# Kernel tuning notes

Measured on AMD Instinct MI355X. Metric: run time of the kernel, lower is better.

Reference implementation:

```python
import jax, jax.numpy as jnp
import numpy as np

VTH = 1.0          # firing threshold
SG_ALPHA = 4.0     # surrogate-gradient sharpness
TAU_MEM = 20.0

@jax.custom_vjp
def spike_fn(v):
    # Heaviside spike: 1 where membrane exceeds 0 (v is already v_mem - VTH)
    return (v > 0.0).astype(v.dtype)

def _spike_fwd(v):
    return spike_fn(v), v

def _spike_bwd(v, g):
    # sigmoid surrogate derivative: alpha * s * (1 - s)
    s = jax.nn.sigmoid(SG_ALPHA * v)
    return (g * SG_ALPHA * s * (1.0 - s),)

spike_fn.defvjp(_spike_fwd, _spike_bwd)

def lif_scan(h):
    # h: (batch, time, seq, hidden) -> spikes same shape, rate scalar
    beta = 1.0 - 1.0 / TAU_MEM  # membrane decay
    b, t, s, d = h.shape
    h_t = jnp.moveaxis(h, 1, 0)  # (time, batch, seq, hidden)

    def step(v, inp):
        v = beta * v + inp
        spk = spike_fn(v - VTH)
        v = v * (1.0 - spk)  # hard reset
        return v, spk

    v0 = jnp.zeros((b, s, d), dtype=h.dtype)
    _, spikes = jax.lax.scan(step, v0, h_t)
    spikes = jnp.moveaxis(spikes, 0, 1)  # (batch, time, seq, hidden)
    rate = spikes.mean()
    return spikes, rate

def setup_inputs() -> dict:
    key = jax.random.key(0)
    k1, k2, k3 = jax.random.split(key, 3)
    b, t, s, d = 16, 4, 256, 512
    hidden = 2048
    x = jax.random.normal(k1, (b, t, s, d), dtype=jnp.float32)
    # Kaiming-ish init so membrane inputs are O(1)
    w1 = jax.random.normal(k2, (hidden, d), dtype=jnp.float32) * (1.0 / np.sqrt(d))
    w2 = jax.random.normal(k3, (d, hidden), dtype=jnp.float32) * (1.0 / np.sqrt(hidden))
    return {"x": x, "w1": w1, "w2": w2}

def reference(x, w1, w2):
    # fc1: (b,t,s,d) @ (hidden,d)^T -> (b,t,s,hidden)
    h = jnp.einsum('btsd,hd->btsh', x, w1)
    spikes, rate = lif_scan(h)
    # fc2: (b,t,s,hidden) @ (d,hidden)^T -> (b,t,s,d)
    out = jnp.einsum('btsh,dh->btsd', spikes, w2)
    return out, rate
```

## Files before the change

kernel.cpp:

```cpp
#include <hip/hip_runtime.h>
#include <stdint.h>


typedef __attribute__((ext_vector_type(8))) short short8;
typedef __attribute__((ext_vector_type(4))) float f32x4;

#define AS1 __attribute__((address_space(1)))
#define AS3 __attribute__((address_space(3)))

__device__ __forceinline__ void load_lds16(const void* g, void* l) {
  __builtin_amdgcn_global_load_lds((const AS1 void*)g, (AS3 void*)l, 16, 0, 0);
}

__device__ __forceinline__ unsigned short f2bf(float f) {
  union { float f; unsigned u; } un; un.f = f;
  unsigned r = un.u + 0x7FFF + ((un.u >> 16) & 1);
  return (unsigned short)(r >> 16);
}
__device__ __forceinline__ float bf2f(unsigned short u) {
  union { unsigned u; float f; } un; un.u = ((unsigned)u) << 16; return un.f;
}

__global__ __launch_bounds__(256) void k0_split(
    const float* __restrict__ w2, unsigned short* __restrict__ hi,
    unsigned short* __restrict__ lo)
{
  int i = (blockIdx.x * 256 + threadIdx.x) * 4;
  float4 w = *(const float4*)&w2[i];
  unsigned short h4[4], l4[4];
  float ws[4] = {w.x, w.y, w.z, w.w};
#pragma unroll
  for (int c = 0; c < 4; ++c) {
    unsigned short h = f2bf(ws[c]);
    h4[c] = h;
    l4[c] = f2bf(ws[c] - bf2f(h));
  }
  *(ushort4*)&hi[i] = *(const ushort4*)h4;
  *(ushort4*)&lo[i] = *(const ushort4*)l4;
}

#define K1KT 32
#define SA_STR 256
#define SB_STR 128

__global__ __launch_bounds__(256, 2) void k1_gemm_lif(
    const float* __restrict__ x,
    const float* __restrict__ w1,
    unsigned short* __restrict__ spikes,
    unsigned* __restrict__ cnt_out)
{
  __shared__ float sA[K1KT * SA_STR];
  __shared__ float sB[K1KT * SB_STR];

  const int tid = threadIdx.x;
  const int tx  = tid & 15;
  const int ty  = tid >> 4;
  const int t   = ty & 3;
  const int ssg = ty >> 2;

  const int bx = blockIdx.x;
  const int b  = bx >> 2;
  const int s0 = (bx & 3) * 64;
  const int h0 = blockIdx.y * 128;

  const int u  = tid >> 3;
  const int kg = tid & 7;

  float acc[16][8];
#pragma unroll
  for (int i = 0; i < 16; ++i)
#pragma unroll
    for (int j = 0; j < 8; ++j) acc[i][j] = 0.0f;

  const int aBase  = t * 64 + ssg * 16;
  const int tXor   = 4 * t;
  const int bBase0 = tx * 4;
  const int bBase1 = 64 + tx * 4;

  for (int k0 = 0; k0 < 512; k0 += K1KT) {
    __syncthreads();

#pragma unroll
    for (int j = 0; j < 8; ++j) {
      int r  = u + 32 * j;
      int tr = r >> 6, ss = r & 63;
      size_t grow = ((size_t)(b * 4 + tr) << 8) + s0 + ss;
      float4 a = *(const float4*)&x[grow * 512 + k0 + kg * 4];
      int sl = r ^ (4 * (kg ^ tr));
      sA[(4 * kg + 0) * SA_STR + sl] = a.x;
      sA[(4 * kg + 1) * SA_STR + sl] = a.y;
      sA[(4 * kg + 2) * SA_STR + sl] = a.z;
      sA[(4 * kg + 3) * SA_STR + sl] = a.w;
    }
#pragma unroll
    for (int j = 0; j < 4; ++j) {
      int c = u + 32 * j;
      float4 wv = *(const float4*)&w1[(size_t)(h0 + c) * 512 + k0 + kg * 4];
      int sl = c ^ (4 * kg);
      sB[(4 * kg + 0) * SB_STR + sl] = wv.x;
      sB[(4 * kg + 1) * SB_STR + sl] = wv.y;
      sB[(4 * kg + 2) * SB_STR + sl] = wv.z;
      sB[(4 * kg + 3) * SB_STR + sl] = wv.w;
    }
    __syncthreads();

    for (int kk = 0; kk < K1KT; kk += 4) {
      const int aXor = kk ^ tXor;
      const int bXor = kk;
#pragma unroll
      for (int k2i = 0; k2i < 4; ++k2i) {
        const int k = kk + k2i;
        const float* aRow = &sA[k * SA_STR];
        const float* bRow = &sB[k * SB_STR];
        float4 a0 = *(const float4*)&aRow[(aBase + 0)  ^ aXor];
        float4 a1 = *(const float4*)&aRow[(aBase + 4)  ^ aXor];
        float4 a2 = *(const float4*)&aRow[(aBase + 8)  ^ aXor];
        float4 a3 = *(const float4*)&aRow[(aBase + 12) ^ aXor];
        float4 b0 = *(const float4*)&bRow[bBase0 ^ bXor];
        float4 b1 = *(const float4*)&bRow[bBase1 ^ bXor];
        float av[16] = {a0.x, a0.y, a0.z, a0.w, a1.x, a1.y, a1.z, a1.w,
                        a2.x, a2.y, a2.z, a2.w, a3.x, a3.y, a3.z, a3.w};
        float bv[8]  = {b0.x, b0.y, b0.z, b0.w, b1.x, b1.y, b1.z, b1.w};
#pragma unroll
        for (int i = 0; i < 16; ++i)
#pragma unroll
          for (int j = 0; j < 8; ++j)
            acc[i][j] = __builtin_fmaf(av[i], bv[j], acc[i][j]);
      }
    }
  }

  unsigned cnt = 0;
#pragma unroll
  for (int i = 0; i < 16; ++i) {
    unsigned short sp[8];
#pragma unroll
    for (int j = 0; j < 8; ++j) {
      float a = acc[i][j];
      float h[4];
#pragma unroll
      for (int tt = 0; tt < 4; ++tt)
        h[tt] = __shfl(a, tt * 16 + tx, 64);
      float vv = 0.0f;
      bool smine = false;
#pragma unroll
      for (int tt = 0; tt < 4; ++tt) {
        vv = __fadd_rn(__fmul_rn(0.95f, vv), h[tt]);
        bool s = vv > 1.0f;
        smine = (tt == t) ? s : smine;
        vv = s ? 0.0f : vv;
      }
      cnt += smine ? 1u : 0u;
      sp[j] = smine ? (unsigned short)0x3F80 : (unsigned short)0;
    }
    size_t grow = ((size_t)(b * 4 + t) << 8) + s0 + ssg * 16 + i;
    unsigned short* rowp = spikes + grow * 2048 + h0;
    *(ushort4*)&rowp[tx * 4]      = *(const ushort4*)&sp[0];
    *(ushort4*)&rowp[64 + tx * 4] = *(const ushort4*)&sp[4];
  }

#pragma unroll
  for (int off = 32; off; off >>= 1) cnt += __shfl_down(cnt, off);
  if ((tid & 63) == 0) atomicAdd(cnt_out, cnt);
}

__global__ __launch_bounds__(256, 2) void k2_gemm_mfma(
    const unsigned short* __restrict__ spikes,
    const unsigned short* __restrict__ w2h,
    const unsigned short* __restrict__ w2l,
    float* __restrict__ out)
{
  __shared__ alignas(16) short smA [128 * 64];
  __shared__ alignas(16) short smBh[128 * 64];
  __shared__ alignas(16) short smBl[128 * 64];

  const int tid  = threadIdx.x;
  const int lane = tid & 63;
  const int quad = lane >> 4;
  const int l15  = lane & 15;
  const int wv   = tid >> 6;
  const int wm   = wv & 1;
  const int wn   = wv >> 1;

  const size_t r0 = (size_t)blockIdx.x * 128;
  const int    d0 = blockIdx.y * 128;

  int srow[4], sg8[4];
#pragma unroll
  for (int j = 0; j < 4; ++j) {
    int gi  = j * 256 + tid;
    srow[j] = gi >> 3;
    sg8[j]  = ((gi & 7) ^ (srow[j] & 7)) * 8;
  }

  const unsigned short* ab  = spikes + r0 * 2048;
  const unsigned short* bhb = w2h + (size_t)d0 * 2048;
  const unsigned short* blb = w2l + (size_t)d0 * 2048;

  f32x4 acc[4][4] = {};

  for (int k0 = 0; k0 < 2048; k0 += 64) {
    __syncthreads();
#pragma unroll
    for (int j = 0; j < 4; ++j) {
      load_lds16(ab  + (size_t)srow[j] * 2048 + k0 + sg8[j],
                 &smA [(j * 256 + tid) * 8]);
      load_lds16(bhb + (size_t)srow[j] * 2048 + k0 + sg8[j],
                 &smBh[(j * 256 + tid) * 8]);
      load_lds16(blb + (size_t)srow[j] * 2048 + k0 + sg8[j],
                 &smBl[(j * 256 + tid) * 8]);
    }
    __syncthreads();

#pragma unroll
    for (int ks = 0; ks < 2; ++ks) {
      short8 af[4], bh[4], bl[4];
#pragma unroll
      for (int mi = 0; mi < 4; ++mi) {
        int m = wm * 64 + mi * 16 + l15;
        af[mi] = ((const short8*)smA)[m * 8 + ((ks * 4 + quad) ^ (m & 7))];
      }
#pragma unroll
      for (int ni = 0; ni < 4; ++ni) {
        int n = wn * 64 + ni * 16 + l15;
        int sl = n * 8 + ((ks * 4 + quad) ^ (n & 7));
        bh[ni] = ((const short8*)smBh)[sl];
        bl[ni] = ((const short8*)smBl)[sl];
      }
#pragma unroll
      for (int mi = 0; mi < 4; ++mi)
#pragma unroll
        for (int ni = 0; ni < 4; ++ni) {
          acc[mi][ni] = __builtin_amdgcn_mfma_f32_16x16x32_bf16(
              af[mi], bh[ni], acc[mi][ni], 0, 0, 0);
          acc[mi][ni] = __builtin_amdgcn_mfma_f32_16x16x32_bf16(
              af[mi], bl[ni], acc[mi][ni], 0, 0, 0);
        }
    }
  }

  float* ob = out + r0 * 512 + d0;
#pragma unroll
  for (int mi = 0; mi < 4; ++mi)
#pragma unroll
    for (int ni = 0; ni < 4; ++ni)
#pragma unroll
      for (int r = 0; r < 4; ++r) {
        int rr = wm * 64 + mi * 16 + quad * 4 + r;
        int cc = wn * 64 + ni * 16 + l15;
        ob[(size_t)rr * 512 + cc] = acc[mi][ni][r];
      }
}

#define KT 16
#define PADF 68

__global__ __launch_bounds__(256) void k2_gemm_valu(
    const unsigned short* __restrict__ spikes,
    const float* __restrict__ w2,
    float* __restrict__ out)
{
  __shared__ float sA[KT][PADF];
  __shared__ float sB[KT][PADF];

  const int tid = threadIdx.x;
  const int tx  = tid & 15;
  const int ty  = tid >> 4;
  const int lr  = tid >> 2;
  const int lg  = tid & 3;

  const size_t r0 = (size_t)blockIdx.x * 64;
  const int    d0 = blockIdx.y * 64;

  float acc[4][4];
#pragma unroll
  for (int i = 0; i < 4; ++i)
#pragma unroll
    for (int j = 0; j < 4; ++j) acc[i][j] = 0.0f;

  for (int k0 = 0; k0 < 2048; k0 += KT) {
    __syncthreads();
    ushort4 av = *(const ushort4*)&spikes[(r0 + lr) * 2048 + k0 + lg * 4];
    float4  bv = *(const float4*)&w2[(size_t)(d0 + lr) * 2048 + k0 + lg * 4];
    sA[lg * 4 + 0][lr] = bf2f(av.x); sA[lg * 4 + 1][lr] = bf2f(av.y);
    sA[lg * 4 + 2][lr] = bf2f(av.z); sA[lg * 4 + 3][lr] = bf2f(av.w);
    sB[lg * 4 + 0][lr] = bv.x; sB[lg * 4 + 1][lr] = bv.y;
    sB[lg * 4 + 2][lr] = bv.z; sB[lg * 4 + 3][lr] = bv.w;
    __syncthreads();

#pragma unroll
    for (int k = 0; k < KT; ++k) {
      float4 a4 = *(const float4*)&sA[k][ty * 4];
      float4 b4 = *(const float4*)&sB[k][tx * 4];
      float aa[4] = {a4.x, a4.y, a4.z, a4.w};
      float bb[4] = {b4.x, b4.y, b4.z, b4.w};
#pragma unroll
      for (int i = 0; i < 4; ++i)
#pragma unroll
        for (int j = 0; j < 4; ++j)
          acc[i][j] = __builtin_fmaf(aa[i], bb[j], acc[i][j]);
    }
  }

#pragma unroll
  for (int i = 0; i < 4; ++i) {
    float4 o = make_float4(acc[i][0], acc[i][1], acc[i][2], acc[i][3]);
    *(float4*)&out[(r0 + ty * 4 + i) * 512 + d0 + tx * 4] = o;
  }
}

__global__ void k3_rate(const unsigned* __restrict__ cnt, float* __restrict__ dst) {
  dst[0] = (float)((double)(*cnt) / 33554432.0);
}

extern "C" void kernel_launch(void* const* d_in, const int* in_sizes, int n_in,
                              void* d_out, int out_size, void* d_ws, size_t ws_size,
                              hipStream_t stream) {
  const float* x  = (const float*)d_in[0];
  const float* w1 = (const float*)d_in[1];
  const float* w2 = (const float*)d_in[2];
  float* out = (float*)d_out;

  unsigned* cnt = (unsigned*)d_ws;
  unsigned short* spikes = (unsigned short*)((char*)d_ws + 256);
  const size_t SPIKES_B = (size_t)16384 * 2048 * 2;
  unsigned short* w2h = (unsigned short*)((char*)d_ws + 256 + SPIKES_B);
  unsigned short* w2l = w2h + (size_t)512 * 2048;
  const size_t NEED_SPLIT = 256 + SPIKES_B + 2 * (size_t)512 * 2048 * 2;

  hipMemsetAsync(d_ws, 0, 256, stream);

  hipLaunchKernelGGL(k1_gemm_lif, dim3(64, 16), dim3(256), 0, stream,
                     x, w1, spikes, cnt);

  if (ws_size >= NEED_SPLIT) {
    hipLaunchKernelGGL(k0_split, dim3(1024), dim3(256), 0, stream, w2, w2h, w2l);
    hipLaunchKernelGGL(k2_gemm_mfma, dim3(128, 4), dim3(256), 0, stream,
                       spikes, w2h, w2l, out);
  } else {
    hipLaunchKernelGGL(k2_gemm_valu, dim3(256, 8), dim3(256), 0, stream,
                       spikes, w2, out);
  }

  hipLaunchKernelGGL(k3_rate, dim3(1), dim3(1), 0, stream, cnt, out + 8388608);
}
```

Baseline: 562.6 us.

## Pre-transpose x and w1 so fc1 tiles load directly into LDS

```diff
diff --git a/kernel.cpp b/kernel.cpp
--- a/kernel.cpp
+++ b/kernel.cpp
@@ -21,6 +21,29 @@
   union { unsigned u; float f; } un; un.u = ((unsigned)u) << 16; return un.f;
 }
 
+__global__ __launch_bounds__(256) void ktrans(
+    const float* __restrict__ s, float* __restrict__ d, int M, int N)
+{
+  __shared__ float t[64][68];
+  const int tx = threadIdx.x & 15, ty = threadIdx.x >> 4;
+  const size_t r0 = (size_t)blockIdx.x * 64;
+  const int    c0 = blockIdx.y * 64;
+#pragma unroll
+  for (int p = 0; p < 4; ++p) {
+    int r = ty + 16 * p;
+    float4 v = *(const float4*)&s[(r0 + r) * N + c0 + tx * 4];
+    t[tx * 4 + 0][r] = v.x; t[tx * 4 + 1][r] = v.y;
+    t[tx * 4 + 2][r] = v.z; t[tx * 4 + 3][r] = v.w;
+  }
+  __syncthreads();
+#pragma unroll
+  for (int p = 0; p < 4; ++p) {
+    int c = ty + 16 * p;
+    float4 v = *(const float4*)&t[c][tx * 4];
+    *(float4*)&d[(size_t)(c0 + c) * M + r0 + tx * 4] = v;
+  }
+}
+
 __global__ __launch_bounds__(256) void k0_split(
     const float* __restrict__ w2, unsigned short* __restrict__ hi,
     unsigned short* __restrict__ lo)
@@ -40,14 +63,126 @@
 }
 
 #define K1KT 32
+
+__global__ __launch_bounds__(256, 2) void k1_gemm_lif(
+    const float* __restrict__ xT,
+    const float* __restrict__ w1T,
+    unsigned short* __restrict__ spikes,
+    unsigned* __restrict__ cnt_out)
+{
+  __shared__ float sA[K1KT * 256];
+  __shared__ float sB[K1KT * 128];
+
+  const int tid  = threadIdx.x;
+  const int lane = tid & 63;
+  const int w    = tid >> 6;
+  const int tx   = tid & 15;
+  const int ty   = tid >> 4;
+  const int t    = ty & 3;
+  const int ssg  = ty >> 2;
+
+  const int bx = blockIdx.x;
+  const int b  = bx >> 2;
+  const int s0 = (bx & 3) * 64;
+  const int h0 = blockIdx.y * 128;
+
+  const int aT = lane >> 4;
+  const int aS = (lane & 15) * 4;
+  const int bK = lane >> 5;
+  const int bC = (lane & 31) * 4;
+
+  const float* aSrc = xT + ((size_t)(b * 4 + aT) << 8) + s0 + aS;
+  const float* bSrc = w1T + h0 + bC;
+
+  float acc[16][8];
+#pragma unroll
+  for (int i = 0; i < 16; ++i)
+#pragma unroll
+    for (int j = 0; j < 8; ++j) acc[i][j] = 0.0f;
+
+  const int aBase = t * 64 + ssg * 16;
+
+  for (int k0 = 0; k0 < 512; k0 += K1KT) {
+    __syncthreads();
+
+#pragma unroll
+    for (int j = 0; j < 8; ++j) {
+      int kr = w * 8 + j;
+      load_lds16(aSrc + (size_t)(k0 + kr) * 16384, &sA[kr * 256 + lane * 4]);
+    }
+#pragma unroll
+    for (int j = 0; j < 4; ++j) {
+      int kr = (w * 4 + j) * 2;
+      load_lds16(bSrc + (size_t)(k0 + kr + bK) * 2048,
+                 &sB[kr * 128 + lane * 4]);
+    }
+    __syncthreads();
+
+#pragma unroll
+    for (int k = 0; k < K1KT; ++k) {
+      const float* aRow = &sA[k * 256];
+      const float* bRow = &sB[k * 128];
+      float4 afr[4];
+#pragma unroll
+      for (int ig = 0; ig < 4; ++ig) {
+        int igr = (ig + t) & 3;
+        afr[igr] = *(const float4*)&aRow[aBase + 4 * igr];
+      }
+      float4 b0 = *(const float4*)&bRow[tx * 4];
+      float4 b1 = *(const float4*)&bRow[64 + tx * 4];
+      float av[16] = {afr[0].x, afr[0].y, afr[0].z, afr[0].w,
+                      afr[1].x, afr[1].y, afr[1].z, afr[1].w,
+                      afr[2].x, afr[2].y, afr[2].z, afr[2].w,
+                      afr[3].x, afr[3].y, afr[3].z, afr[3].w};
+      float bv[8]  = {b0.x, b0.y, b0.z, b0.w, b1.x, b1.y, b1.z, b1.w};
+#pragma unroll
+      for (int i = 0; i < 16; ++i)
+#pragma unroll
+        for (int j = 0; j < 8; ++j)
+          acc[i][j] = __builtin_fmaf(av[i], bv[j], acc[i][j]);
+    }
+  }
+
+  unsigned cnt = 0;
+#pragma unroll
+  for (int i = 0; i < 16; ++i) {
+    unsigned short sp[8];
+#pragma unroll
+    for (int j = 0; j < 8; ++j) {
+      float a = acc[i][j];
+      float h[4];
+#pragma unroll
+      for (int tt = 0; tt < 4; ++tt)
+        h[tt] = __shfl(a, tt * 16 + tx, 64);
+      float vv = 0.0f;
+      bool smine = false;
+#pragma unroll
+      for (int tt = 0; tt < 4; ++tt) {
+        vv = __fadd_rn(__fmul_rn(0.95f, vv), h[tt]);
+        bool s = vv > 1.0f;
+        smine = (tt == t) ? s : smine;
+        vv = s ? 0.0f : vv;
+      }
+      cnt += smine ? 1u : 0u;
+      sp[j] = smine ? (unsigned short)0x3F80 : (unsigned short)0;
+    }
+    size_t grow = ((size_t)(b * 4 + t) << 8) + s0 + ssg * 16 + i;
+    unsigned short* rowp = spikes + grow * 2048 + h0;
+    *(ushort4*)&rowp[tx * 4]      = *(const ushort4*)&sp[0];
+    *(ushort4*)&rowp[64 + tx * 4] = *(const ushort4*)&sp[4];
+  }
+
+#pragma unroll
+  for (int off = 32; off; off >>= 1) cnt += __shfl_down(cnt, off);
+  if ((tid & 63) == 0) atomicAdd(cnt_out, cnt);
+}
+
 #define SA_STR 256
 #define SB_STR 128
 
-__global__ __launch_bounds__(256, 2) void k1_gemm_lif(
-    const float* __restrict__ x,
-    const float* __restrict__ w1,
-    unsigned short* __restrict__ spikes,
-    unsigned* __restrict__ cnt_out)
+__global__ __launch_bounds__(256, 2) void k1_fb(
+    const float* __restrict__ x, const float* __restrict__ w1,
+    unsigned short* __restrict__ spikes, unsigned* __restrict__ cnt_out)
 {
   __shared__ float sA[K1KT * SA_STR];
   __shared__ float sB[K1KT * SB_STR];
@@ -79,7 +214,6 @@
 
   for (int k0 = 0; k0 < 512; k0 += K1KT) {
     __syncthreads();
-
 #pragma unroll
     for (int j = 0; j < 8; ++j) {
       int r  = u + 32 * j;
@@ -321,17 +455,33 @@
   const float* w2 = (const float*)d_in[2];
   float* out = (float*)d_out;
 
-  unsigned* cnt = (unsigned*)d_ws;
-  unsigned short* spikes = (unsigned short*)((char*)d_ws + 256);
+  char* wsb = (char*)d_ws;
+  unsigned* cnt = (unsigned*)wsb;
+  unsigned short* spikes = (unsigned short*)(wsb + 256);
   const size_t SPIKES_B = (size_t)16384 * 2048 * 2;
-  unsigned short* w2h = (unsigned short*)((char*)d_ws + 256 + SPIKES_B);
+  const size_t W2S_B    = (size_t)512 * 2048 * 2;
+  unsigned short* w2h = (unsigned short*)(wsb + 256 + SPIKES_B);
   unsigned short* w2l = w2h + (size_t)512 * 2048;
-  const size_t NEED_SPLIT = 256 + SPIKES_B + 2 * (size_t)512 * 2048 * 2;
+  float* xT  = (float*)(wsb + 256 + SPIKES_B + 2 * W2S_B);
+  float* w1T = xT + (size_t)512 * 16384;
+
+  const size_t NEED_SPLIT = 256 + SPIKES_B + 2 * W2S_B;
+  const size_t NEED_ALL   = NEED_SPLIT + (size_t)512 * 16384 * 4
+                                       + (size_t)512 * 2048 * 4;
 
   hipMemsetAsync(d_ws, 0, 256, stream);
 
-  hipLaunchKernelGGL(k1_gemm_lif, dim3(64, 16), dim3(256), 0, stream,
-                     x, w1, spikes, cnt);
+  if (ws_size >= NEED_ALL) {
+    hipLaunchKernelGGL(ktrans, dim3(256, 8), dim3(256), 0, stream,
+                       x, xT, 16384, 512);
+    hipLaunchKernelGGL(ktrans, dim3(32, 8), dim3(256), 0, stream,
+                       w1, w1T, 2048, 512);
+    hipLaunchKernelGGL(k1_gemm_lif, dim3(64, 16), dim3(256), 0, stream,
+                       xT, w1T, spikes, cnt);
+  } else {
+    hipLaunchKernelGGL(k1_fb, dim3(64, 16), dim3(256), 0, stream,
+                       x, w1, spikes, cnt);
+  }
 
   if (ws_size >= NEED_SPLIT) {
     hipLaunchKernelGGL(k0_split, dim3(1024), dim3(256), 0, stream, w2, w2h, w2l);
```

After: 2.036 ms. +261.9%, slower.
